# Kernel optimization log

Measured on AMD Instinct MI355X. Metric: run time of the kernel, lower is better.

## Reference

```python
import jax, jax.numpy as jnp
import numpy as np
import math

B, SEQ, PRED, NVAR, NMARK = 32, 512, 96, 862, 4
DM, DS, DFF, NL, DCONV = 512, 16, 512, 4, 2
DTR = math.ceil(DM / 16)  # mamba dt_rank = 32
EPS = 1e-5


def setup_inputs() -> dict:
    key = jax.random.key(0)
    ks = iter(jax.random.split(key, 48))
    rn = lambda shape, s=0.02: jax.random.normal(next(ks), shape, jnp.float32) * s
    inp = {
        "x_enc": jax.random.normal(next(ks), (B, SEQ, NVAR), jnp.float32),
        "x_mark_enc": jax.random.normal(next(ks), (B, SEQ, NMARK), jnp.float32),
        "x_dec": jax.random.normal(next(ks), (B, 144, NVAR), jnp.float32),
        "x_mark_dec": jax.random.normal(next(ks), (B, 144, NMARK), jnp.float32),
        # inverted embedding: Linear(seq_len -> d_model)
        "W_emb": rn((DM, SEQ)), "b_emb": jnp.zeros((DM,), jnp.float32),
        # per layer, 2 directional Mamba blocks (expand=1 -> d_inner = DM)
        "m_Win": rn((NL, 2, 2 * DM, DM)),
        "m_convw": rn((NL, 2, DM, DCONV), 0.2),
        "m_convb": jnp.zeros((NL, 2, DM), jnp.float32),
        "m_Wx": rn((NL, 2, DTR + 2 * DS, DM)),
        "m_Wdt": rn((NL, 2, DM, DTR), 0.1),
        "m_bdt": jnp.full((NL, 2, DM), -4.0, jnp.float32),
        "m_Alog": jnp.log(jnp.broadcast_to(jnp.arange(1, DS + 1, dtype=jnp.float32), (NL, 2, DM, DS))) + 0.0,
        "m_D": jnp.ones((NL, 2, DM), jnp.float32),
        "m_Wout": rn((NL, 2, DM, DM)),
        # position-wise FFN (Conv1d k=1 == Linear)
        "W1": rn((NL, DFF, DM)), "b1": jnp.zeros((NL, DFF), jnp.float32),
        "W2": rn((NL, DM, DFF)), "b2": jnp.zeros((NL, DM), jnp.float32),
        "ln1_g": jnp.ones((NL, DM), jnp.float32), "ln1_b": jnp.zeros((NL, DM), jnp.float32),
        "ln2_g": jnp.ones((NL, DM), jnp.float32), "ln2_b": jnp.zeros((NL, DM), jnp.float32),
        "lnf_g": jnp.ones((DM,), jnp.float32), "lnf_b": jnp.zeros((DM,), jnp.float32),
        "head_W": rn((PRED, DM)), "head_b": jnp.zeros((PRED,), jnp.float32),
        "train": 0,
    }
    return inp


def _ln(x, g, b):
    mu = x.mean(-1, keepdims=True)
    var = x.var(-1, keepdims=True)
    return (x - mu) * jax.lax.rsqrt(var + EPS) * g + b


def _mamba(u, Win, convw, convb, Wx, Wdt, bdt, Alog, Dp, Wout):
    # u: [B, L, DM] -> [B, L, DM]; selective scan (mamba_ssm semantics)
    Bsz, L, _ = u.shape
    xz = jnp.einsum('bld,ed->ble', u, Win)          # [B,L,2*DM]
    x, z = jnp.split(xz, 2, axis=-1)
    # depthwise causal conv, kernel size DCONV=2
    xp = jnp.pad(x, ((0, 0), (DCONV - 1, 0), (0, 0)))
    x = sum(xp[:, i:i + L] * convw[:, i] for i in range(DCONV)) + convb
    x = jax.nn.silu(x)
    dbc = jnp.einsum('bld,ed->ble', x, Wx)          # [B,L,DTR+2*DS]
    dt = jax.nn.softplus(jnp.einsum('blr,dr->bld', dbc[..., :DTR], Wdt) + bdt)  # [B,L,DM]
    Bm = dbc[..., DTR:DTR + DS]                      # [B,L,DS]
    Cm = dbc[..., DTR + DS:]                         # [B,L,DS]
    A = -jnp.exp(Alog)                               # [DM,DS]

    def step(h, inp):
        dt_t, B_t, C_t, x_t = inp                    # [B,DM],[B,DS],[B,DS],[B,DM]
        dA = jnp.exp(dt_t[..., None] * A)            # [B,DM,DS]
        h = dA * h + (dt_t * x_t)[..., None] * B_t[:, None, :]
        y = jnp.einsum('bds,bs->bd', h, C_t)
        return h, y

    h0 = jnp.zeros((Bsz, DM, DS), u.dtype)
    xs = (dt.transpose(1, 0, 2), Bm.transpose(1, 0, 2), Cm.transpose(1, 0, 2), x.transpose(1, 0, 2))
    _, ys = jax.lax.scan(step, h0, xs)               # ys: [L,B,DM]
    y = ys.transpose(1, 0, 2) + Dp * x
    y = y * jax.nn.silu(z)
    return jnp.einsum('bld,od->blo', y, Wout)


def _forward(x_enc, x_mark_enc, W_emb, b_emb, m_Win, m_convw, m_convb, m_Wx, m_Wdt,
             m_bdt, m_Alog, m_D, m_Wout, W1, b1, W2, b2, ln1_g, ln1_b, ln2_g, ln2_b,
             lnf_g, lnf_b, head_W, head_b):
    means = jax.lax.stop_gradient(x_enc.mean(1, keepdims=True))
    xc = x_enc - means
    stdev = jnp.sqrt(xc.var(1, keepdims=True) + EPS)   # unbiased=False
    xn = xc / stdev
    # inverted embedding: tokens = variates (+ time-mark channels)
    tok = jnp.concatenate([xn.transpose(0, 2, 1), x_mark_enc.transpose(0, 2, 1)], 1)  # [B, N+M, SEQ]
    h = jnp.einsum('bns,ds->bnd', tok, W_emb) + b_emb                                 # [B, N+M, DM]
    for l in range(NL):
        fwd = _mamba(h, m_Win[l, 0], m_convw[l, 0], m_convb[l, 0], m_Wx[l, 0],
                     m_Wdt[l, 0], m_bdt[l, 0], m_Alog[l, 0], m_D[l, 0], m_Wout[l, 0])
        rev = _mamba(h[:, ::-1], m_Win[l, 1], m_convw[l, 1], m_convb[l, 1], m_Wx[l, 1],
                     m_Wdt[l, 1], m_bdt[l, 1], m_Alog[l, 1], m_D[l, 1], m_Wout[l, 1])[:, ::-1]
        h = _ln(h + fwd + rev, ln1_g[l], ln1_b[l])
        y = jax.nn.gelu(jnp.einsum('bnd,fd->bnf', h, W1[l]) + b1[l], approximate=False)
        y = jnp.einsum('bnf,df->bnd', y, W2[l]) + b2[l]
        h = _ln(h + y, ln2_g[l], ln2_b[l])
    h = _ln(h, lnf_g, lnf_b)
    dec = jnp.einsum('bnd,pd->bnp', h, head_W) + head_b    # [B, N+M, PRED]
    dec = dec.transpose(0, 2, 1)[:, :, :NVAR]              # [B, PRED, N]
    dec = dec * stdev[:, 0:1, :] + means[:, 0:1, :]
    return dec[:, -PRED:, :]


def reference(x_enc, x_mark_enc, x_dec, x_mark_dec, W_emb, b_emb, m_Win, m_convw,
              m_convb, m_Wx, m_Wdt, m_bdt, m_Alog, m_D, m_Wout, W1, b1, W2, b2,
              ln1_g, ln1_b, ln2_g, ln2_b, lnf_g, lnf_b, head_W, head_b, train):
    dec = _forward(x_enc, x_mark_enc, W_emb, b_emb, m_Win, m_convw, m_convb, m_Wx,
                   m_Wdt, m_bdt, m_Alog, m_D, m_Wout, W1, b1, W2, b2, ln1_g, ln1_b,
                   ln2_g, ln2_b, lnf_g, lnf_b, head_W, head_b)
    loss_reg = jnp.float32(0.0)  # regularizer inactive in eval (train=False)
    return dec, loss_reg
```

## Files before the change

kernel.cpp:

```cpp
#include <hip/hip_runtime.h>
#include <hip/hip_bf16.h>
#include <cmath>

typedef __bf16 bf;
typedef _Float16 fp16;
typedef __bf16 bfrag __attribute__((ext_vector_type(8)));
typedef __bf16 bf4 __attribute__((ext_vector_type(4)));
typedef _Float16 h4 __attribute__((ext_vector_type(4)));
typedef float  f32x4 __attribute__((ext_vector_type(4)));

constexpr int BSZ = 32, SEQ = 512, NVAR = 862, NMARK = 4, NTOK = 866;
constexpr int DM = 512, DS = 16, DTR = 32, DFF = 512, NL = 4, PRED = 96;
constexpr int M = BSZ * NTOK;
constexpr float EPS = 1e-5f;
constexpr int NCH = 64, CL = 14;
static_assert(NCH * CL >= NTOK, "chunks must cover sequence");

__device__ __forceinline__ void gload16(const void* g, void* l) {
    __builtin_amdgcn_global_load_lds((const __attribute__((address_space(1))) void*)g,
                                     (__attribute__((address_space(3))) void*)l, 16, 0, 0);
}

__global__ void cvt_kernel(const float* __restrict__ src, bf* __restrict__ dst, int n4) {
    int i = blockIdx.x * 256 + threadIdx.x;
    if (i >= n4) return;
    f32x4 v = ((const f32x4*)src)[i];
    bf o[4];
    o[0] = (bf)v[0]; o[1] = (bf)v[1]; o[2] = (bf)v[2]; o[3] = (bf)v[3];
    *(uint2*)&dst[i * 4] = *(uint2*)o;
}

__global__ void fold_kernel(const float* __restrict__ Wdt, const float* __restrict__ Wx,
                            bf* __restrict__ out) {
    int idx = blockIdx.x * 256 + threadIdx.x;
    int k = idx & 511; int rest = idx >> 9;
    int row = rest % 544; int ld = rest / 544;
    float s;
    if (row < 512) {
        const float* wd = Wdt + ((size_t)ld * 512 + row) * 32;
        const float* wx = Wx + (size_t)ld * 64 * 512 + k;
        s = 0.f;
#pragma unroll 8
        for (int r = 0; r < 32; r++) s += wd[r] * wx[(size_t)r * 512];
    } else {
        s = Wx[(size_t)ld * 64 * 512 + (size_t)(32 + row - 512) * 512 + k];
    }
    out[((size_t)ld * 544 + row) * 512 + k] = (bf)s;
}

__global__ __launch_bounds__(256) void meanstd_kernel(const float* __restrict__ xe,
                               float* __restrict__ mean, float* __restrict__ stdv) {
    __shared__ float sm[2][4][64];
    int b = blockIdx.y;
    int vl = threadIdx.x & 63;
    int tg = threadIdx.x >> 6;
    int v = blockIdx.x * 64 + vl;
    float s = 0.f, sq = 0.f;
    if (v < NVAR) {
        const float* p = xe + (size_t)b * SEQ * NVAR + (size_t)tg * 128 * NVAR + v;
#pragma unroll 4
        for (int t = 0; t < 128; t++) {
            float x = p[(size_t)t * NVAR];
            s += x; sq += x * x;
        }
    }
    sm[0][tg][vl] = s; sm[1][tg][vl] = sq;
    __syncthreads();
    if (tg == 0 && v < NVAR) {
        s  = sm[0][0][vl] + sm[0][1][vl] + sm[0][2][vl] + sm[0][3][vl];
        sq = sm[1][0][vl] + sm[1][1][vl] + sm[1][2][vl] + sm[1][3][vl];
        float mu = s * (1.f / SEQ);
        float var = sq * (1.f / SEQ) - mu * mu;
        mean[b * NVAR + v] = mu;
        stdv[b * NVAR + v] = sqrtf(var + EPS);
    }
}

__global__ void tok_kernel(const float* __restrict__ xe, const float* __restrict__ xm,
                           const float* __restrict__ mean, const float* __restrict__ stdv,
                           bf* __restrict__ tok) {
    __shared__ float tile[32][33];
    int b = blockIdx.z;
    int v0 = blockIdx.x * 32, s0 = blockIdx.y * 32;
    int tx = threadIdx.x, ty = threadIdx.y;
    int v = v0 + tx;
    float mu = 0.f, rs = 0.f;
    if (v < NVAR) { mu = mean[b * NVAR + v]; rs = 1.f / stdv[b * NVAR + v]; }
#pragma unroll
    for (int j = 0; j < 4; j++) {
        int s = s0 + ty + j * 8;
        float val = 0.f;
        if (v < NVAR)       val = (xe[((size_t)b * SEQ + s) * NVAR + v] - mu) * rs;
        else if (v < NTOK)  val = xm[((size_t)b * SEQ + s) * NMARK + (v - NVAR)];
        tile[ty + j * 8][tx] = val;
    }
    __syncthreads();
#pragma unroll
    for (int j = 0; j < 4; j++) {
        int n = v0 + ty + j * 8;
        if (n < NTOK)
            tok[((size_t)b * NTOK + n) * SEQ + s0 + tx] = (bf)tile[tx][ty + j * 8];
    }
}

template <int BN, int ACT, bool BIAS, bool RES, bool HEAD, bool DTBC, typename CT>
__global__ __launch_bounds__(512, 4) void gemm_kernel(
    const bf* __restrict__ A0, const bf* __restrict__ A1,
    const bf* __restrict__ W0, const bf* __restrict__ W1,
    CT* __restrict__ C, float* __restrict__ C2,
    const float* __restrict__ bias, const bf* __restrict__ res,
    int Mreal, int Nreal, int K, int lda, int ldw, int ksplit, int ldc,
    size_t sAz, size_t sWz, size_t sCz, size_t sC2z, size_t sBiasz,
    const float* __restrict__ mean, const float* __restrict__ stdv) {
    constexpr int BM = 128, BK = 64;
    static_assert(BN == 128, "8-wave layout assumes 128x128 tile");
    constexpr int NT = 2;
    __shared__ __align__(16) bf Als[2][BM * BK];
    __shared__ __align__(16) bf Bls[2][BN * BK];

    int gx = gridDim.x, gy = gridDim.y;
    int gxy = gx * gy;
    int nbt = gxy * gridDim.z;
    int id = blockIdx.x + gx * (blockIdx.y + gy * blockIdx.z);
    int q8 = nbt >> 3, r8 = nbt & 7;
    int xcd = id & 7, rank = id >> 3;
    int w = xcd * q8 + (xcd < r8 ? xcd : r8) + rank;
    int z = w / gxy;
    int rem = w - z * gxy;
    int m0 = (rem / gy) * BM;
    int n0 = (rem % gy) * BN;

    A0 += (size_t)z * sAz; W0 += (size_t)z * sWz; C += (size_t)z * sCz;
    if (DTBC) C2 += (size_t)z * sC2z;
    if (BIAS) bias += (size_t)z * sBiasz;
    int tid = threadIdx.x, lane = tid & 63, wave = tid >> 6;
    int wm = wave >> 2, wn = wave & 3;
    int q = lane >> 4, ml = lane & 15;
    int srow = lane >> 3;
    int aswz = ((lane & 7) ^ srow) * 8;
    int swz = ((q ^ (ml & 7))) * 8;

    f32x4 acc[4][NT];
#pragma unroll
    for (int i = 0; i < 4; i++)
#pragma unroll
        for (int j = 0; j < NT; j++) { acc[i][j][0] = 0.f; acc[i][j][1] = 0.f; acc[i][j][2] = 0.f; acc[i][j][3] = 0.f; }

    auto stage = [&](int kt, int buf) {
        const bf* ab = (ksplit && kt >= ksplit) ? (A1 + (kt - ksplit)) : (A0 + kt);
        const bf* wb = (ksplit && kt >= ksplit) ? (W1 + (kt - ksplit)) : (W0 + kt);
#pragma unroll
        for (int i = 0; i < 2; i++) {
            int r = wave * 16 + i * 8;
            gload16(ab + (size_t)(m0 + r + srow) * lda + aswz, &Als[buf][r * BK]);
        }
#pragma unroll
        for (int i = 0; i < 2; i++) {
            int r = wave * 16 + i * 8;
            gload16(wb + (size_t)(n0 + r + srow) * ldw + aswz, &Bls[buf][r * BK]);
        }
    };

    stage(0, 0);
    int cur = 0;
    for (int kt = 0; kt < K; kt += BK) {
        bool pf = (kt + BK < K);
        if (pf) stage(kt + BK, cur ^ 1);
        if (pf) asm volatile("s_waitcnt vmcnt(4)" ::: "memory");
        else    asm volatile("s_waitcnt vmcnt(0)" ::: "memory");
        __builtin_amdgcn_s_barrier();
        __builtin_amdgcn_sched_barrier(0);
#pragma unroll
        for (int kk = 0; kk < BK; kk += 32) {
            bfrag af[4], bff[NT];
#pragma unroll
            for (int i = 0; i < 4; i++)
                af[i] = *(bfrag*)&Als[cur][(wm * 64 + i * 16 + ml) * BK + (swz ^ kk)];
#pragma unroll
            for (int j = 0; j < NT; j++)
                bff[j] = *(bfrag*)&Bls[cur][(wn * 32 + j * 16 + ml) * BK + (swz ^ kk)];
#pragma unroll
            for (int i = 0; i < 4; i++)
#pragma unroll
                for (int j = 0; j < NT; j++)
                    acc[i][j] = __builtin_amdgcn_mfma_f32_16x16x32_bf16(bff[j], af[i], acc[i][j], 0, 0, 0);
        }
        __builtin_amdgcn_sched_barrier(0);
        __builtin_amdgcn_s_barrier();
        cur ^= 1;
    }

#pragma unroll
    for (int i = 0; i < 4; i++) {
        int row = m0 + wm * 64 + i * 16 + ml;
        if (row >= Mreal) continue;
#pragma unroll
        for (int j = 0; j < NT; j++) {
            int colb = n0 + wn * 32 + j * 16 + q * 4;
            if (colb >= Nreal) continue;
            f32x4 x = acc[i][j];
            if constexpr (BIAS) {
                if (!DTBC || colb < 512) {
                    f32x4 bv = *(const f32x4*)&bias[colb];
#pragma unroll
                    for (int r = 0; r < 4; r++) x[r] += bv[r];
                }
            }
            if constexpr (DTBC) {
                if (colb < 512) {
                    h4 hv;
#pragma unroll
                    for (int r = 0; r < 4; r++) {
                        float xs = (x[r] > 20.f) ? x[r] : __logf(1.f + __expf(x[r]));
                        hv[r] = (_Float16)xs;
                    }
                    *(h4*)&C[(size_t)row * 512 + colb] = hv;
                } else {
                    *(f32x4*)&C2[(size_t)row * 32 + (colb - 512)] = x;
                }
            } else {
                if constexpr (ACT == 1) {
#pragma unroll
                    for (int r = 0; r < 4; r++)
                        x[r] = 0.5f * x[r] * (1.f + erff(x[r] * 0.70710678118654752f));
                }
                if constexpr (RES) {
                    bf4 rv = *(const bf4*)&res[(size_t)row * DM + colb];
#pragma unroll
                    for (int r = 0; r < 4; r++) x[r] += (float)rv[r];
                }
                if constexpr (HEAD) {
                    int bidx = row / NTOK, n = row - bidx * NTOK;
                    if (n < NVAR) {
                        float sc = stdv[bidx * NVAR + n], mm = mean[bidx * NVAR + n];
#pragma unroll
                        for (int r = 0; r < 4; r++) {
                            int col = colb + r;
                            if (col < Nreal)
                                C[((size_t)bidx * PRED + col) * NVAR + n] = (CT)(x[r] * sc + mm);
                        }
                    }
                } else {
                    bf4 ov;
#pragma unroll
                    for (int r = 0; r < 4; r++) ov[r] = (bf)x[r];
                    *(bf4*)&C[(size_t)row * ldc + colb] = ov;
                }
            }
        }
    }
    if (HEAD && blockIdx.x == 0 && blockIdx.y == 0 && blockIdx.z == 0 && tid == 0)
        C[(size_t)BSZ * PRED * NVAR] = (CT)0.f;
}

__global__ void conv_kernel(const bf* __restrict__ xz, const float* __restrict__ cw,
                            const float* __restrict__ cb, bf* __restrict__ xc, int Mc) {
    int id = blockIdx.x * 256 + threadIdx.x;
    int dir = id / (Mc * 64); int rem = id - dir * (Mc * 64);
    int token = rem >> 6; int ch0 = (rem & 63) * 8;
    int t = token % NTOK;
    const bf* xb = xz + (size_t)token * (4 * DM) + dir * (2 * DM) + ch0;
    bfrag xt = *(const bfrag*)xb;
    bfrag xn;
#pragma unroll
    for (int i = 0; i < 8; i++) xn[i] = (bf)0.f;
    int tn = dir ? t + 1 : t - 1;
    if ((unsigned)tn < (unsigned)NTOK)
        xn = *(const bfrag*)(xb + (dir ? (4 * DM) : -(4 * DM)));
    const float2* cwp = (const float2*)cw + ((size_t)dir * DM + ch0);
    const float*  cbp = cb + (size_t)dir * DM + ch0;
    bfrag ov;
#pragma unroll
    for (int jj = 0; jj < 8; jj++) {
        float2 w = cwp[jj];
        float x = (float)xn[jj] * w.x + (float)xt[jj] * w.y + cbp[jj];
        x = x / (1.f + __expf(-x));
        ov[jj] = (bf)x;
    }
    *(bfrag*)(xc + (size_t)dir * Mc * DM + (size_t)token * DM + ch0) = ov;
}

template <bool FINAL>
__global__ __launch_bounds__(256) void scan_chunk_kernel(
    const fp16* __restrict__ dtc, const float* __restrict__ dbc,
    const bf* __restrict__ xc, const bf* __restrict__ xz,
    const float* __restrict__ Alog, const float* __restrict__ Dp,
    float* __restrict__ hloc, float* __restrict__ dtsums,
    bf* __restrict__ y, int Mc) {
    __shared__ __align__(16) float row[4][32];
    int wid = threadIdx.x >> 6;
    int lane = threadIdx.x & 63;
    int dg = blockIdx.x * 4 + wid, b = blockIdx.y;
    int zc = blockIdx.z; int dir = zc / NCH, c = zc - dir * NCH;
    int d = dg * 64 + lane;
    int dd = dir * DM + d;
    float A2[16];
    {
        const f32x4* ap = (const f32x4*)(Alog + (size_t)dd * DS);
#pragma unroll
        for (int i = 0; i < 4; i++) {
            f32x4 v = ap[i];
#pragma unroll
            for (int jj = 0; jj < 4; jj++)
                A2[i * 4 + jj] = -__expf(v[jj]) * 1.4426950408889634f;
        }
    }
    float A20 = A2[0];
    bool lc = true;
#pragma unroll
    for (int s = 1; s < 16; s++)
        lc = lc && (fabsf(A2[s] - (s + 1) * A20) <= 1e-4f * fabsf(A2[s]));
    bool fast = (__ballot(lc) == ~0ull);
    float Dd = FINAL ? Dp[dd] : 0.f;

    const size_t gbase = ((((size_t)b * 2 + dir) * 8 + dg) * NCH + c);
    const size_t sbase = gbase * 1024 + lane;
    float h[16];
#pragma unroll
    for (int s = 0; s < 16; s++) h[s] = FINAL ? hloc[sbase + (size_t)s * 64] : 0.f;
    float dtsum = 0.f;

    const int t0 = c * CL;
    const int t1e = (t0 + CL < NTOK) ? t0 + CL : NTOK;
    const long step = dir ? -1 : 1;

    const fp16* dtp = nullptr; const float* bcp = nullptr;
    const bf* xcp = nullptr; const bf* xzp = nullptr; bf* yp = nullptr;
    float dtq = 0.f; f32x4 gq = {0.f, 0.f, 0.f, 0.f}; bf xq = (bf)0.f, zq = (bf)0.f;
    if (t0 < t1e) {
        long tok0 = (long)b * NTOK + (dir ? (NTOK - 1 - t0) : t0);
        dtp = dtc + (size_t)dir * Mc * 512 + (size_t)tok0 * 512 + d;
        bcp = dbc + ((size_t)dir * Mc + (size_t)tok0) * 32;
        xcp = xc + (size_t)dir * Mc * 512 + (size_t)tok0 * 512 + d;
        dtq = (float)*dtp;
        if (lane < 8) gq = ((const f32x4*)bcp)[lane];
        xq = *xcp;
        if (FINAL) {
            xzp = xz + (size_t)tok0 * 2048 + dir * 1024 + 512 + d;
            yp  = y  + (size_t)tok0 * 1024 + dir * 512 + d;
            zq = *xzp;
        }
    }
    const long sdt = step * 512, sbc = step * 32, sxc = step * 512;
    const long sxz = step * 2048, sy = step * 1024;

    for (int t = t0; t < t1e; t++) {
        if (lane < 8) ((f32x4*)row[wid])[lane] = gq;
        float dt = dtq;
        float x = (float)xq;
        float zv = (float)zq;
        bf* ypc = yp;
        if (t + 1 < t1e) {
            dtp += sdt; bcp += sbc; xcp += sxc;
            dtq = (float)*dtp;
            if (lane < 8) gq = ((const f32x4*)bcp)[lane];
            xq = *xcp;
            if (FINAL) { xzp += sxz; zq = *xzp; yp += sy; }
        }
        const f32x4* rv = (const f32x4*)row[wid];
        float dtx = dt * x;
        dtsum += dt;
        float yv0 = 0.f, yv1 = 0.f, yv2 = 0.f, yv3 = 0.f;
        if (fast) {
            float r  = exp2f(dt * A20);
            float r2 = r * r, r3 = r2 * r, r4 = r2 * r2;
            float bse = r;
#pragma unroll
            for (int i = 0; i < 4; i++) {
                f32x4 Bv = rv[i];
                f32x4 Cv = rv[4 + i];
                float p0 = bse, p1 = bse * r, p2 = bse * r2, p3 = bse * r3;
                int s = i * 4;
                h[s + 0] = p0 * h[s + 0] + dtx * Bv[0];
                h[s + 1] = p1 * h[s + 1] + dtx * Bv[1];
                h[s + 2] = p2 * h[s + 2] + dtx * Bv[2];
                h[s + 3] = p3 * h[s + 3] + dtx * Bv[3];
                if (FINAL) {
                    yv0 += Cv[0] * h[s + 0];
                    yv1 += Cv[1] * h[s + 1];
                    yv2 += Cv[2] * h[s + 2];
                    yv3 += Cv[3] * h[s + 3];
                }
                bse *= r4;
            }
        } else {
#pragma unroll
            for (int i = 0; i < 4; i++) {
                f32x4 Bv = rv[i];
                f32x4 Cv = rv[4 + i];
#pragma unroll
                for (int jj = 0; jj < 4; jj++) {
                    int s = i * 4 + jj;
                    float a = exp2f(dt * A2[s]);
                    h[s] = a * h[s] + dtx * Bv[jj];
                    if (FINAL) yv0 += Cv[jj] * h[s];
                }
            }
        }
        if (FINAL) {
            float yv = (yv0 + yv1) + (yv2 + yv3);
            float sz = zv / (1.f + __expf(-zv));
            *ypc = (bf)((yv + Dd * x) * sz);
        }
    }
    if (!FINAL) {
#pragma unroll
        for (int s = 0; s < 16; s++) hloc[sbase + (size_t)s * 64] = h[s];
        dtsums[gbase * 64 + lane] = dtsum;
    }
}

__global__ void scan_fix_kernel(float* __restrict__ hloc, const float* __restrict__ dtsums,
                                const float* __restrict__ Alog, int total) {
    int tid = blockIdx.x * 256 + threadIdx.x;
    if (tid >= total) return;
    int lane = tid & 63;
    int s = (tid >> 6) & 15;
    int g = tid >> 10;
    int dg = g & 7, dir = (g >> 3) & 1;
    int dd = dir * DM + dg * 64 + lane;
    float A2s = -__expf(Alog[(size_t)dd * DS + s]) * 1.4426950408889634f;
    size_t i0 = (((size_t)g * NCH) * 16 + s) * 64 + lane;
    size_t d0 = ((size_t)g * NCH) * 64 + lane;
    float H = 0.f;
#pragma unroll 8
    for (int c = 0; c < NCH; c++) {
        size_t ix = i0 + (size_t)c * 1024;
        float hl = hloc[ix];
        float ap = exp2f(dtsums[d0 + (size_t)c * 64] * A2s);
        hloc[ix] = H;
        H = hl + ap * H;
    }
}

__global__ __launch_bounds__(256) void ln_kernel(const bf* X, bf* Y,
                                                 const float* __restrict__ g, const float* __restrict__ bb) {
    int token = blockIdx.x * 4 + (threadIdx.x >> 6);
    int lane = threadIdx.x & 63;
    bfrag xv = *(const bfrag*)(X + (size_t)token * DM + lane * 8);
    float xf[8]; float s = 0.f, sq = 0.f;
#pragma unroll
    for (int j = 0; j < 8; j++) { xf[j] = (float)xv[j]; s += xf[j]; sq += xf[j] * xf[j]; }
#pragma unroll
    for (int o = 1; o < 64; o <<= 1) { s += __shfl_xor(s, o); sq += __shfl_xor(sq, o); }
    float mu = s * (1.f / DM);
    float rs = rsqrtf(sq * (1.f / DM) - mu * mu + EPS);
    f32x4 g0 = ((const f32x4*)g)[lane * 2], g1 = ((const f32x4*)g)[lane * 2 + 1];
    f32x4 b0 = ((const f32x4*)bb)[lane * 2], b1 = ((const f32x4*)bb)[lane * 2 + 1];
    bfrag ov;
#pragma unroll
    for (int j = 0; j < 8; j++) {
        float gg = (j < 4) ? g0[j] : g1[j - 4];
        float bbv = (j < 4) ? b0[j] : b1[j - 4];
        ov[j] = (bf)((xf[j] - mu) * rs * gg + bbv);
    }
    *(bfrag*)(Y + (size_t)token * DM + lane * 8) = ov;
}

extern "C" void kernel_launch(void* const* d_in, const int* in_sizes, int n_in,
                              void* d_out, int out_size, void* d_ws, size_t ws_size,
                              hipStream_t stream) {
    const float* x_enc = (const float*)d_in[0];
    const float* x_mark = (const float*)d_in[1];
    const float* W_emb = (const float*)d_in[4];
    const float* b_emb = (const float*)d_in[5];
    const float* mWin = (const float*)d_in[6];
    const float* mcw = (const float*)d_in[7];
    const float* mcb = (const float*)d_in[8];
    const float* mWx = (const float*)d_in[9];
    const float* mWdt = (const float*)d_in[10];
    const float* mbdt = (const float*)d_in[11];
    const float* mAlog = (const float*)d_in[12];
    const float* mD = (const float*)d_in[13];
    const float* mWout = (const float*)d_in[14];
    const float* W1w = (const float*)d_in[15];
    const float* b1w = (const float*)d_in[16];
    const float* W2w = (const float*)d_in[17];
    const float* b2w = (const float*)d_in[18];
    const float* ln1g = (const float*)d_in[19];
    const float* ln1b = (const float*)d_in[20];
    const float* ln2g = (const float*)d_in[21];
    const float* ln2b = (const float*)d_in[22];
    const float* lnfg = (const float*)d_in[23];
    const float* lnfb = (const float*)d_in[24];
    const float* headW = (const float*)d_in[25];
    const float* headb = (const float*)d_in[26];

    auto a256 = [](size_t x) { return (x + 255) & ~(size_t)255; };
    char* ws = (char*)d_ws;
    size_t off = 0;
    auto alloc = [&](size_t n) { size_t r = off; off += a256(n); return ws + r; };
    float* mean = (float*)alloc((size_t)BSZ * NVAR * 4);
    float* stdv = (float*)alloc((size_t)BSZ * NVAR * 4);
    bf* h  = (bf*)alloc((size_t)M * DM * 2);
    bf* t1 = (bf*)alloc((size_t)M * DM * 2);
    bf* t2 = (bf*)alloc((size_t)M * DM * 2);
    constexpr int nEmb = 512 * 512, nWin = NL * 2 * 1024 * 512,
                  nWout = NL * 2 * 512 * 512, nW1 = NL * DFF * DM, nW2 = NL * DM * DFF,
                  nHead = PRED * DM, nComb = NL * 2 * 544 * 512;
    bf* wEmb  = (bf*)alloc((size_t)nEmb * 2);
    bf* wWin  = (bf*)alloc((size_t)nWin * 2);
    bf* wWout = (bf*)alloc((size_t)nWout * 2);
    bf* wW1   = (bf*)alloc((size_t)nW1 * 2);
    bf* wW2   = (bf*)alloc((size_t)nW2 * 2);
    bf* wHead = (bf*)alloc((size_t)nHead * 2);
    bf* wComb = (bf*)alloc((size_t)nComb * 2);
    size_t fixedEnd = off;

    auto scanScr = [&](size_t cb) { return cb * 2 * 8 * (size_t)NCH * 16 * 64 * 4; };
    auto dtsScr  = [&](size_t cb) { return cb * 2 * 8 * (size_t)NCH * 64 * 4; };
    int CB = 1;
    {
        int cbs[6] = {32, 16, 8, 4, 2, 1};
        for (int i = 0; i < 6; i++) {
            size_t mc = (size_t)cbs[i] * NTOK;
            size_t chunkB = a256(mc * 4096) + a256(mc * 2048) + a256(mc * 256)
                          + a256(mc * 2048) + a256(mc * 2048)
                          + a256(scanScr(cbs[i])) + a256(dtsScr(cbs[i]));
            if (fixedEnd + chunkB <= ws_size) { CB = cbs[i]; break; }
        }
    }
    const size_t Mc = (size_t)CB * NTOK;
    size_t co = fixedEnd;
    bf* xzc = (bf*)(ws + co);        co += a256(Mc * 4096);
    bf* xcc = (bf*)(ws + co);        co += a256(Mc * 2048);
    float* dbcc = (float*)(ws + co); co += a256(Mc * 256);
    bf* ycc = (bf*)(ws + co);        co += a256(Mc * 2048);
    fp16* dtcc = (fp16*)(ws + co);   co += a256(Mc * 2048);
    float* hloc = (float*)(ws + co); co += a256(scanScr(CB));
    float* dtsums = (float*)(ws + co);
    const int NC = BSZ / CB;
    const int MTc = (int)((Mc + 127) / 128);
    constexpr int MT = (M + 127) / 128;
    const int fixTotal = CB * 2 * 8 * 16 * 64;

    cvt_kernel<<<(nEmb / 4 + 255) / 256, 256, 0, stream>>>(W_emb, wEmb, nEmb / 4);
    cvt_kernel<<<(nWin / 4 + 255) / 256, 256, 0, stream>>>(mWin, wWin, nWin / 4);
    cvt_kernel<<<(nWout / 4 + 255) / 256, 256, 0, stream>>>(mWout, wWout, nWout / 4);
    cvt_kernel<<<(nW1 / 4 + 255) / 256, 256, 0, stream>>>(W1w, wW1, nW1 / 4);
    cvt_kernel<<<(nW2 / 4 + 255) / 256, 256, 0, stream>>>(W2w, wW2, nW2 / 4);
    cvt_kernel<<<(nHead / 4 + 255) / 256, 256, 0, stream>>>(headW, wHead, nHead / 4);
    fold_kernel<<<(nComb + 255) / 256, 256, 0, stream>>>(mWdt, mWx, wComb);

    meanstd_kernel<<<dim3(14, BSZ), 256, 0, stream>>>(x_enc, mean, stdv);
    tok_kernel<<<dim3(28, 16, BSZ), dim3(32, 8), 0, stream>>>(x_enc, x_mark, mean, stdv, t1);
    gemm_kernel<128, 0, true, false, false, false, bf><<<dim3(MT, 4), 512, 0, stream>>>(
        t1, nullptr, wEmb, nullptr, h, nullptr, b_emb, nullptr,
        M, DM, SEQ, SEQ, SEQ, 0, DM, 0, 0, 0, 0, 0, nullptr, nullptr);

    for (int l = 0; l < NL; l++) {
        const bf* Winl = wWin + (size_t)l * 2 * 1024 * 512;
        const float* cwl = mcw + (size_t)l * 2 * DM * 2;
        const float* cbl = mcb + (size_t)l * 2 * DM;
        const bf* Combl = wComb + (size_t)l * 2 * 544 * 512;
        const float* bdtl = mbdt + (size_t)l * 2 * DM;
        const float* Alogl = mAlog + (size_t)l * 2 * 512 * 16;
        const float* Dl = mD + (size_t)l * 2 * DM;
        const bf* Woutl = wWout + (size_t)l * 2 * 512 * 512;
        const bf* W1l = wW1 + (size_t)l * DFF * DM;
        const bf* W2l = wW2 + (size_t)l * DM * DFF;

        for (int c = 0; c < NC; c++) {
            size_t coff = (size_t)c * Mc;
            gemm_kernel<128, 0, false, false, false, false, bf><<<dim3(MTc, 16), 512, 0, stream>>>(
                h + coff * DM, nullptr, Winl, nullptr, xzc, nullptr, nullptr, nullptr,
                (int)Mc, 2048, 512, 512, 512, 0, 2048, 0, 0, 0, 0, 0, nullptr, nullptr);
            conv_kernel<<<(int)(2 * Mc * 64 / 256), 256, 0, stream>>>(xzc, cwl, cbl, xcc, (int)Mc);
            gemm_kernel<128, 0, true, false, false, true, _Float16><<<dim3(MTc, 5, 2), 512, 0, stream>>>(
                xcc, nullptr, Combl, nullptr, dtcc, dbcc, bdtl, nullptr,
                (int)Mc, 544, 512, 512, 512, 0, 512,
                Mc * 512, (size_t)544 * 512, Mc * 512, Mc * 32, 512, nullptr, nullptr);
            scan_chunk_kernel<false><<<dim3(2, CB, 2 * NCH), 256, 0, stream>>>(
                dtcc, dbcc, xcc, xzc, Alogl, Dl, hloc, dtsums, ycc, (int)Mc);
            scan_fix_kernel<<<(fixTotal + 255) / 256, 256, 0, stream>>>(hloc, dtsums, Alogl, fixTotal);
            scan_chunk_kernel<true><<<dim3(2, CB, 2 * NCH), 256, 0, stream>>>(
                dtcc, dbcc, xcc, xzc, Alogl, Dl, hloc, dtsums, ycc, (int)Mc);
            gemm_kernel<128, 0, false, true, false, false, bf><<<dim3(MTc, 4), 512, 0, stream>>>(
                ycc, ycc + 512, Woutl, Woutl + 512 * 512, t1 + coff * DM, nullptr, nullptr, h + coff * DM,
                (int)Mc, DM, 1024, 1024, 512, 512, DM, 0, 0, 0, 0, 0, nullptr, nullptr);
        }
        ln_kernel<<<M / 4, 256, 0, stream>>>(t1, t2, ln1g + l * DM, ln1b + l * DM);
        gemm_kernel<128, 1, true, false, false, false, bf><<<dim3(MT, 4), 512, 0, stream>>>(
            t2, nullptr, W1l, nullptr, t1, nullptr, b1w + l * DFF, nullptr,
            M, DFF, DM, DM, DM, 0, DFF, 0, 0, 0, 0, 0, nullptr, nullptr);
        gemm_kernel<128, 0, true, true, false, false, bf><<<dim3(MT, 4), 512, 0, stream>>>(
            t1, nullptr, W2l, nullptr, h, nullptr, b2w + l * DM, t2,
            M, DM, DFF, DFF, DFF, 0, DM, 0, 0, 0, 0, 0, nullptr, nullptr);
        ln_kernel<<<M / 4, 256, 0, stream>>>(h, h, ln2g + l * DM, ln2b + l * DM);
    }

    ln_kernel<<<M / 4, 256, 0, stream>>>(h, t1, lnfg, lnfb);
    gemm_kernel<128, 0, true, false, true, false, float><<<dim3(MT, 1), 512, 0, stream>>>(
        t1, nullptr, wHead, nullptr, (float*)d_out, nullptr, headb, nullptr,
        M, PRED, DM, DM, DM, 0, 1, 0, 0, 0, 0, 0, mean, stdv);
}
```

Measured before the change: 3.148 ms.

## Process four channels per thread in chunked selective scan with vectorized I/O

```diff
diff --git a/kernel.cpp b/kernel.cpp
--- a/kernel.cpp
+++ b/kernel.cpp
@@ -281,44 +281,60 @@
 }
 
 template <bool FINAL>
-__global__ __launch_bounds__(256) void scan_chunk_kernel(
+__global__ __launch_bounds__(128, 2) void scan_chunk_kernel(
     const fp16* __restrict__ dtc, const float* __restrict__ dbc,
     const bf* __restrict__ xc, const bf* __restrict__ xz,
     const float* __restrict__ Alog, const float* __restrict__ Dp,
     float* __restrict__ hloc, float* __restrict__ dtsums,
     bf* __restrict__ y, int Mc) {
-    __shared__ __align__(16) float row[4][32];
+    __shared__ __align__(16) float row[2][32];
     int wid = threadIdx.x >> 6;
     int lane = threadIdx.x & 63;
-    int dg = blockIdx.x * 4 + wid, b = blockIdx.y;
-    int zc = blockIdx.z; int dir = zc / NCH, c = zc - dir * NCH;
-    int d = dg * 64 + lane;
-    int dd = dir * DM + d;
-    float A2[16];
-    {
-        const f32x4* ap = (const f32x4*)(Alog + (size_t)dd * DS);
+    int b = blockIdx.x;
+    int zc = blockIdx.y; int dir = zc / NCH, c = zc - dir * NCH;
+    int d0 = wid * 256 + lane * 4;
+    int dd0 = dir * DM + d0;
+
+    constexpr float L2E = 1.4426950408889634f;
+    float A20[4];
+    bool lc = true;
+#pragma unroll
+    for (int cc = 0; cc < 4; cc++) {
+        const f32x4* ap = (const f32x4*)(Alog + (size_t)(dd0 + cc) * DS);
+        float a2[16];
 #pragma unroll
         for (int i = 0; i < 4; i++) {
             f32x4 v = ap[i];
 #pragma unroll
             for (int jj = 0; jj < 4; jj++)
-                A2[i * 4 + jj] = -__expf(v[jj]) * 1.4426950408889634f;
-        }
-    }
-    float A20 = A2[0];
-    bool lc = true;
-#pragma unroll
-    for (int s = 1; s < 16; s++)
-        lc = lc && (fabsf(A2[s] - (s + 1) * A20) <= 1e-4f * fabsf(A2[s]));
+                a2[i * 4 + jj] = -__expf(v[jj]) * L2E;
+        }
+        A20[cc] = a2[0];
+#pragma unroll
+        for (int s = 1; s < 16; s++)
+            lc = lc && (fabsf(a2[s] - (s + 1) * a2[0]) <= 1e-4f * fabsf(a2[s]));
+    }
     bool fast = (__ballot(lc) == ~0ull);
-    float Dd = FINAL ? Dp[dd] : 0.f;
-
-    const size_t gbase = ((((size_t)b * 2 + dir) * 8 + dg) * NCH + c);
-    const size_t sbase = gbase * 1024 + lane;
-    float h[16];
-#pragma unroll
-    for (int s = 0; s < 16; s++) h[s] = FINAL ? hloc[sbase + (size_t)s * 64] : 0.f;
-    float dtsum = 0.f;
+    float Dd[4];
+#pragma unroll
+    for (int cc = 0; cc < 4; cc++) Dd[cc] = FINAL ? Dp[dd0 + cc] : 0.f;
+
+    const size_t hbase = ((size_t)(b * 2 + dir) * NCH + c) * 8192;
+    float h[4][16];
+    if (FINAL) {
+#pragma unroll
+        for (int s = 0; s < 16; s++) {
+            f32x4 hv = *(const f32x4*)&hloc[hbase + (size_t)s * 512 + d0];
+#pragma unroll
+            for (int cc = 0; cc < 4; cc++) h[cc][s] = hv[cc];
+        }
+    } else {
+#pragma unroll
+        for (int cc = 0; cc < 4; cc++)
+#pragma unroll
+            for (int s = 0; s < 16; s++) h[cc][s] = 0.f;
+    }
+    float dtsum[4] = {0.f, 0.f, 0.f, 0.f};
 
     const int t0 = c * CL;
     const int t1e = (t0 + CL < NTOK) ? t0 + CL : NTOK;
@@ -326,19 +342,23 @@
 
     const fp16* dtp = nullptr; const float* bcp = nullptr;
     const bf* xcp = nullptr; const bf* xzp = nullptr; bf* yp = nullptr;
-    float dtq = 0.f; f32x4 gq = {0.f, 0.f, 0.f, 0.f}; bf xq = (bf)0.f, zq = (bf)0.f;
+    h4 dtq = {(_Float16)0.f, (_Float16)0.f, (_Float16)0.f, (_Float16)0.f};
+    bf4 xq; bf4 zq;
+#pragma unroll
+    for (int cc = 0; cc < 4; cc++) { xq[cc] = (bf)0.f; zq[cc] = (bf)0.f; }
+    f32x4 gq = {0.f, 0.f, 0.f, 0.f};
     if (t0 < t1e) {
         long tok0 = (long)b * NTOK + (dir ? (NTOK - 1 - t0) : t0);
-        dtp = dtc + (size_t)dir * Mc * 512 + (size_t)tok0 * 512 + d;
+        dtp = dtc + (size_t)dir * Mc * 512 + (size_t)tok0 * 512 + d0;
         bcp = dbc + ((size_t)dir * Mc + (size_t)tok0) * 32;
-        xcp = xc + (size_t)dir * Mc * 512 + (size_t)tok0 * 512 + d;
-        dtq = (float)*dtp;
+        xcp = xc + (size_t)dir * Mc * 512 + (size_t)tok0 * 512 + d0;
+        dtq = *(const h4*)dtp;
         if (lane < 8) gq = ((const f32x4*)bcp)[lane];
-        xq = *xcp;
+        xq = *(const bf4*)xcp;
         if (FINAL) {
-            xzp = xz + (size_t)tok0 * 2048 + dir * 1024 + 512 + d;
-            yp  = y  + (size_t)tok0 * 1024 + dir * 512 + d;
-            zq = *xzp;
+            xzp = xz + (size_t)tok0 * 2048 + dir * 1024 + 512 + d0;
+            yp  = y  + (size_t)tok0 * 1024 + dir * 512 + d0;
+            zq = *(const bf4*)xzp;
         }
     }
     const long sdt = step * 512, sbc = step * 32, sxc = step * 512;
@@ -346,42 +366,50 @@
 
     for (int t = t0; t < t1e; t++) {
         if (lane < 8) ((f32x4*)row[wid])[lane] = gq;
-        float dt = dtq;
-        float x = (float)xq;
-        float zv = (float)zq;
+        float dtv[4], xv[4], zv[4], dtx[4];
+#pragma unroll
+        for (int cc = 0; cc < 4; cc++) {
+            dtv[cc] = (float)dtq[cc];
+            xv[cc] = (float)xq[cc];
+            if (FINAL) zv[cc] = (float)zq[cc];
+            dtx[cc] = dtv[cc] * xv[cc];
+            dtsum[cc] += dtv[cc];
+        }
         bf* ypc = yp;
         if (t + 1 < t1e) {
             dtp += sdt; bcp += sbc; xcp += sxc;
-            dtq = (float)*dtp;
+            dtq = *(const h4*)dtp;
             if (lane < 8) gq = ((const f32x4*)bcp)[lane];
-            xq = *xcp;
-            if (FINAL) { xzp += sxz; zq = *xzp; yp += sy; }
+            xq = *(const bf4*)xcp;
+            if (FINAL) { xzp += sxz; zq = *(const bf4*)xzp; yp += sy; }
         }
         const f32x4* rv = (const f32x4*)row[wid];
-        float dtx = dt * x;
-        dtsum += dt;
-        float yv0 = 0.f, yv1 = 0.f, yv2 = 0.f, yv3 = 0.f;
+        float yva[4] = {0.f, 0.f, 0.f, 0.f};
         if (fast) {
-            float r  = exp2f(dt * A20);
-            float r2 = r * r, r3 = r2 * r, r4 = r2 * r2;
-            float bse = r;
+            float r[4], r2[4], r3[4], r4[4], bse[4];
+#pragma unroll
+            for (int cc = 0; cc < 4; cc++) {
+                r[cc] = exp2f(dtv[cc] * A20[cc]);
+                r2[cc] = r[cc] * r[cc]; r3[cc] = r2[cc] * r[cc]; r4[cc] = r2[cc] * r2[cc];
+                bse[cc] = r[cc];
+            }
 #pragma unroll
             for (int i = 0; i < 4; i++) {
                 f32x4 Bv = rv[i];
                 f32x4 Cv = rv[4 + i];
-                float p0 = bse, p1 = bse * r, p2 = bse * r2, p3 = bse * r3;
-                int s = i * 4;
-                h[s + 0] = p0 * h[s + 0] + dtx * Bv[0];
-                h[s + 1] = p1 * h[s + 1] + dtx * Bv[1];
-                h[s + 2] = p2 * h[s + 2] + dtx * Bv[2];
-                h[s + 3] = p3 * h[s + 3] + dtx * Bv[3];
-                if (FINAL) {
-                    yv0 += Cv[0] * h[s + 0];
-                    yv1 += Cv[1] * h[s + 1];
-                    yv2 += Cv[2] * h[s + 2];
-                    yv3 += Cv[3] * h[s + 3];
+#pragma unroll
+                for (int cc = 0; cc < 4; cc++) {
+                    int s = i * 4;
+                    float p0 = bse[cc], p1 = p0 * r[cc], p2 = p0 * r2[cc], p3 = p0 * r3[cc];
+                    h[cc][s + 0] = p0 * h[cc][s + 0] + dtx[cc] * Bv[0];
+                    h[cc][s + 1] = p1 * h[cc][s + 1] + dtx[cc] * Bv[1];
+                    h[cc][s + 2] = p2 * h[cc][s + 2] + dtx[cc] * Bv[2];
+                    h[cc][s + 3] = p3 * h[cc][s + 3] + dtx[cc] * Bv[3];
+                    if (FINAL)
+                        yva[cc] += Cv[0] * h[cc][s + 0] + Cv[1] * h[cc][s + 1]
+                                 + Cv[2] * h[cc][s + 2] + Cv[3] * h[cc][s + 3];
+                    bse[cc] *= r4[cc];
                 }
-                bse *= r4;
             }
         } else {
 #pragma unroll
@@ -389,24 +417,40 @@
                 f32x4 Bv = rv[i];
                 f32x4 Cv = rv[4 + i];
 #pragma unroll
-                for (int jj = 0; jj < 4; jj++) {
-                    int s = i * 4 + jj;
-                    float a = exp2f(dt * A2[s]);
-                    h[s] = a * h[s] + dtx * Bv[jj];
-                    if (FINAL) yv0 += Cv[jj] * h[s];
+                for (int cc = 0; cc < 4; cc++) {
+#pragma unroll
+                    for (int jj = 0; jj < 4; jj++) {
+                        int s = i * 4 + jj;
+                        float A2 = -__expf(Alog[(size_t)(dd0 + cc) * DS + s]) * L2E;
+                        float a = exp2f(dtv[cc] * A2);
+                        h[cc][s] = a * h[cc][s] + dtx[cc] * Bv[jj];
+                        if (FINAL) yva[cc] += Cv[jj] * h[cc][s];
+                    }
                 }
             }
         }
         if (FINAL) {
-            float yv = (yv0 + yv1) + (yv2 + yv3);
-            float sz = zv / (1.f + __expf(-zv));
-            *ypc = (bf)((yv + Dd * x) * sz);
+            bf4 ov;
+#pragma unroll
+            for (int cc = 0; cc < 4; cc++) {
+                float sz = zv[cc] / (1.f + __expf(-zv[cc]));
+                ov[cc] = (bf)((yva[cc] + Dd[cc] * xv[cc]) * sz);
+            }
+            *(bf4*)ypc = ov;
         }
     }
     if (!FINAL) {
 #pragma unroll
-        for (int s = 0; s < 16; s++) hloc[sbase + (size_t)s * 64] = h[s];
-        dtsums[gbase * 64 + lane] = dtsum;
+        for (int s = 0; s < 16; s++) {
+            f32x4 hv;
+#pragma unroll
+            for (int cc = 0; cc < 4; cc++) hv[cc] = h[cc][s];
+            *(f32x4*)&hloc[hbase + (size_t)s * 512 + d0] = hv;
+        }
+        f32x4 dv; 
+#pragma unroll
+        for (int cc = 0; cc < 4; cc++) dv[cc] = dtsum[cc];
+        *(f32x4*)&dtsums[((size_t)(b * 2 + dir) * NCH + c) * 512 + d0] = dv;
     }
 }
 
@@ -414,20 +458,19 @@
                                 const float* __restrict__ Alog, int total) {
     int tid = blockIdx.x * 256 + threadIdx.x;
     if (tid >= total) return;
-    int lane = tid & 63;
-    int s = (tid >> 6) & 15;
-    int g = tid >> 10;
-    int dg = g & 7, dir = (g >> 3) & 1;
-    int dd = dir * DM + dg * 64 + lane;
-    float A2s = -__expf(Alog[(size_t)dd * DS + s]) * 1.4426950408889634f;
-    size_t i0 = (((size_t)g * NCH) * 16 + s) * 64 + lane;
-    size_t d0 = ((size_t)g * NCH) * 64 + lane;
+    int d = tid & 511;
+    int s = (tid >> 9) & 15;
+    int g = tid >> 13;
+    int dir = g & 1;
+    float A2s = -__expf(Alog[((size_t)(dir * DM + d)) * DS + s]) * 1.4426950408889634f;
+    size_t i0 = (size_t)g * NCH * 8192 + (size_t)s * 512 + d;
+    size_t d0 = (size_t)g * NCH * 512 + d;
     float H = 0.f;
 #pragma unroll 8
     for (int c = 0; c < NCH; c++) {
-        size_t ix = i0 + (size_t)c * 1024;
+        size_t ix = i0 + (size_t)c * 8192;
         float hl = hloc[ix];
-        float ap = exp2f(dtsums[d0 + (size_t)c * 64] * A2s);
+        float ap = exp2f(dtsums[d0 + (size_t)c * 512] * A2s);
         hloc[ix] = H;
         H = hl + ap * H;
     }
@@ -507,8 +550,8 @@
     bf* wComb = (bf*)alloc((size_t)nComb * 2);
     size_t fixedEnd = off;
 
-    auto scanScr = [&](size_t cb) { return cb * 2 * 8 * (size_t)NCH * 16 * 64 * 4; };
-    auto dtsScr  = [&](size_t cb) { return cb * 2 * 8 * (size_t)NCH * 64 * 4; };
+    auto scanScr = [&](size_t cb) { return cb * 2 * (size_t)NCH * 8192 * 4; };
+    auto dtsScr  = [&](size_t cb) { return cb * 2 * (size_t)NCH * 512 * 4; };
     int CB = 1;
     {
         int cbs[6] = {32, 16, 8, 4, 2, 1};
@@ -532,7 +575,7 @@
     const int NC = BSZ / CB;
     const int MTc = (int)((Mc + 127) / 128);
     constexpr int MT = (M + 127) / 128;
-    const int fixTotal = CB * 2 * 8 * 16 * 64;
+    const int fixTotal = CB * 2 * 16 * 512;
 
     cvt_kernel<<<(nEmb / 4 + 255) / 256, 256, 0, stream>>>(W_emb, wEmb, nEmb / 4);
     cvt_kernel<<<(nWin / 4 + 255) / 256, 256, 0, stream>>>(mWin, wWin, nWin / 4);
@@ -570,10 +613,10 @@
                 xcc, nullptr, Combl, nullptr, dtcc, dbcc, bdtl, nullptr,
                 (int)Mc, 544, 512, 512, 512, 0, 512,
                 Mc * 512, (size_t)544 * 512, Mc * 512, Mc * 32, 512, nullptr, nullptr);
-            scan_chunk_kernel<false><<<dim3(2, CB, 2 * NCH), 256, 0, stream>>>(
+            scan_chunk_kernel<false><<<dim3(CB, 2 * NCH), 128, 0, stream>>>(
                 dtcc, dbcc, xcc, xzc, Alogl, Dl, hloc, dtsums, ycc, (int)Mc);
             scan_fix_kernel<<<(fixTotal + 255) / 256, 256, 0, stream>>>(hloc, dtsums, Alogl, fixTotal);
-            scan_chunk_kernel<true><<<dim3(2, CB, 2 * NCH), 256, 0, stream>>>(
+            scan_chunk_kernel<true><<<dim3(CB, 2 * NCH), 128, 0, stream>>>(
                 dtcc, dbcc, xcc, xzc, Alogl, Dl, hloc, dtsums, ycc, (int)Mc);
             gemm_kernel<128, 0, false, true, false, false, bf><<<dim3(MTc, 4), 512, 0, stream>>>(
                 ycc, ycc + 512, Woutl, Woutl + 512 * 512, t1 + coff * DM, nullptr, nullptr, h + coff * DM,
```

Result: no change. 3.088 ms (-1.9%).
